# Performance work log

Measured on AMD Instinct MI355X. Metric: run time of the kernel, lower is better.

Reference implementation:

```python
import jax, jax.numpy as jnp
import numpy as np

N_HEADS = 32
N_KV_HEADS = 8
HEAD_DIM = 128
DIM = 4096
BSZ = 2
SEQLEN = 2048
ROPE_THETA = 500000.0


def setup_inputs() -> dict:
    key = jax.random.key(0)
    ks = jax.random.split(key, 6)
    s = 0.02
    x = jax.random.normal(ks[0], (BSZ, SEQLEN, DIM), dtype=jnp.float32)
    wq = jax.random.normal(ks[1], (N_HEADS * HEAD_DIM, DIM), dtype=jnp.float32) * s
    wk = jax.random.normal(ks[2], (N_KV_HEADS * HEAD_DIM, DIM), dtype=jnp.float32) * s
    wv = jax.random.normal(ks[3], (N_KV_HEADS * HEAD_DIM, DIM), dtype=jnp.float32) * s
    wo = jax.random.normal(ks[4], (DIM, N_HEADS * HEAD_DIM), dtype=jnp.float32) * s
    cache_k = jnp.zeros((BSZ, SEQLEN, N_KV_HEADS, HEAD_DIM), dtype=jnp.float32)
    cache_v = jnp.zeros((BSZ, SEQLEN, N_KV_HEADS, HEAD_DIM), dtype=jnp.float32)
    # rotary frequencies: freqs_cis[t, j] = exp(i * t * theta^(-2j/hd)); pass cos/sin parts
    inv = 1.0 / (ROPE_THETA ** (jnp.arange(0, HEAD_DIM, 2, dtype=jnp.float32) / HEAD_DIM))
    t = jnp.arange(SEQLEN, dtype=jnp.float32)
    ang = jnp.outer(t, inv)  # [S, hd/2]
    freqs_cos = jnp.cos(ang)
    freqs_sin = jnp.sin(ang)
    # causal additive mask
    mask = jnp.triu(jnp.full((SEQLEN, SEQLEN), -jnp.inf, dtype=jnp.float32), k=1)
    return {"x": x, "wq": wq, "wk": wk, "wv": wv, "wo": wo,
            "cache_k": cache_k, "cache_v": cache_v,
            "freqs_cos": freqs_cos, "freqs_sin": freqs_sin,
            "mask": mask, "start_pos": 0}


def _apply_rope(t, cos, sin):
    # t: [B, S, h, hd]; cos/sin: [S, hd/2]
    B, S, h, hd = t.shape
    tf = t.astype(jnp.float32).reshape(B, S, h, hd // 2, 2)
    a, b = tf[..., 0], tf[..., 1]
    c = cos[None, :, None, :]
    s = sin[None, :, None, :]
    out = jnp.stack([a * c - b * s, a * s + b * c], axis=-1)
    return out.reshape(B, S, h, hd).astype(t.dtype)


def reference(x, wq, wk, wv, wo, cache_k, cache_v, freqs_cos, freqs_sin, mask, start_pos):
    B, S, D = x.shape
    hd = HEAD_DIM
    n_rep = N_HEADS // N_KV_HEADS
    xq = (x @ wq.T).reshape(B, S, N_HEADS, hd)
    xk = (x @ wk.T).reshape(B, S, N_KV_HEADS, hd)
    xv = (x @ wv.T).reshape(B, S, N_KV_HEADS, hd)
    xq = _apply_rope(xq, freqs_cos, freqs_sin)
    xk = _apply_rope(xk, freqs_cos, freqs_sin)
    # KV cache write + slice
    cache_k = jax.lax.dynamic_update_slice(cache_k, xk, (0, start_pos, 0, 0))
    cache_v = jax.lax.dynamic_update_slice(cache_v, xv, (0, start_pos, 0, 0))
    kv_len = start_pos + S
    keys = cache_k[:B, :kv_len]    # [B, K, kvh, hd]
    values = cache_v[:B, :kv_len]
    # GQA: repeat kv heads
    keys = jnp.repeat(keys, n_rep, axis=2)     # [B, K, H, hd]
    values = jnp.repeat(values, n_rep, axis=2)
    q = xq.transpose(0, 2, 1, 3)       # [B, H, S, hd]
    k = keys.transpose(0, 2, 1, 3)     # [B, H, K, hd]
    v = values.transpose(0, 2, 1, 3)
    scores = jnp.einsum('bhqd,bhkd->bhqk', q, k) / jnp.sqrt(jnp.float32(hd))
    if mask is not None:
        scores = scores + mask[None, None, :, :]
    probs = jax.nn.softmax(scores.astype(jnp.float32), axis=-1).astype(q.dtype)
    out = jnp.einsum('bhqk,bhkd->bhqd', probs, v)
    out = out.transpose(0, 2, 1, 3).reshape(B, S, N_HEADS * hd)
    return out @ wo.T
```

## Files before the change

### kernel.cpp

```cpp
#include <hip/hip_runtime.h>
#include <hip/hip_bf16.h>
#include <math.h>

typedef __attribute__((ext_vector_type(8)))  __bf16 bfrag;
typedef __attribute__((ext_vector_type(4)))  float  f32x4;
typedef __attribute__((ext_vector_type(16))) float  f32x16;
typedef __attribute__((ext_vector_type(8)))  short  s16x8;
typedef __attribute__((ext_vector_type(4)))  short  s16x4;
typedef __attribute__((ext_vector_type(2)))  unsigned u32x2;
typedef __attribute__((ext_vector_type(4)))  unsigned u32x4;

__device__ __forceinline__ short f2bf(float f) {
  return (short)__builtin_bit_cast(unsigned short, (__bf16)f);
}
__device__ __forceinline__ float bf2f(short s) {
  return (float)__builtin_bit_cast(__bf16, (unsigned short)s);
}
__device__ __forceinline__ unsigned cvtpk(float lo, float hi_) {
  unsigned r;
  asm("v_cvt_pk_bf16_f32 %0, %1, %2" : "=v"(r) : "v"(lo), "v"(hi_));
  return r;
}
__device__ __forceinline__ void gll16(const void* g, void* l) {
  __builtin_amdgcn_global_load_lds((const __attribute__((address_space(1))) void*)g,
                                   (__attribute__((address_space(3))) void*)l, 16, 0, 0);
}

__global__ __launch_bounds__(256) void cvt_f32_bf16(const float* __restrict__ in,
                                                    short* __restrict__ out, int n4) {
  int i = blockIdx.x * 256 + threadIdx.x;
  if (i >= n4) return;
  f32x4 v = ((const f32x4*)in)[i];
  s16x4 o;
  o.x = f2bf(v.x); o.y = f2bf(v.y); o.z = f2bf(v.z); o.w = f2bf(v.w);
  ((s16x4*)out)[i] = o;
}

template<bool BF16OUT>
__global__ __launch_bounds__(512) void gemm256(const short* __restrict__ A,
                                               const short* __restrict__ B,
                                               void* __restrict__ Cv,
                                               int M, int N, int K, int NBX) {
  __shared__ __align__(16) short As[2][256 * 64];
  __shared__ __align__(16) short Bs[2][256 * 64];
  const int tid = threadIdx.x, lane = tid & 63, wid = tid >> 6;
  const int lr = lane & 15, lg = lane >> 4;
  const int wm = wid >> 2, wn = wid & 3;
  const int nwg = gridDim.x, orig = blockIdx.x;
  const int qq = nwg >> 3, rr = nwg & 7, xc = orig & 7, o8 = orig >> 3;
  const int wg = (xc < rr ? xc * (qq + 1) : rr * (qq + 1) + (xc - rr) * qq) + o8;
  const int bm = (wg / NBX) << 8, bn = (wg % NBX) << 8;
  const int NT = K >> 6;
  const int r0 = tid >> 3;
  const int c0 = tid & 7;
  const int csrc = c0 ^ (r0 & 7);

#define STG(OP, OPs, boff, bb, hh, kt_)                                          \
  do {                                                                           \
    _Pragma("unroll")                                                            \
    for (int s = 0; s < 2; ++s)                                                  \
      gll16(OP + (size_t)(boff + (hh) * 128 + s * 64 + r0) * K + (kt_) * 64 + csrc * 8, \
            (char*)OPs[bb] + ((hh) * 128 + s * 64 + wid * 8) * 128);             \
  } while (0)

  int ch[2];
#pragma unroll
  for (int ks = 0; ks < 2; ++ks) ch[ks] = (((ks << 2) | lg) ^ (lr & 7)) << 4;
  const int aoff = (wm * 128 + lr) * 128;
  const int boff_ = (wn * 64 + lr) * 128;

#define RD_A(dst, bb, ih)                                                        \
  do {                                                                           \
    const char* ab = (const char*)As[bb] + aoff + (ih) * 8192;                   \
    _Pragma("unroll") for (int i = 0; i < 4; ++i)                                \
      _Pragma("unroll") for (int ks = 0; ks < 2; ++ks)                           \
        dst[i][ks] = *(const bfrag*)(ab + i * 2048 + ch[ks]);                    \
  } while (0)
#define RD_B(dst, bb, jh)                                                        \
  do {                                                                           \
    const char* bp = (const char*)Bs[bb] + boff_ + (jh) * 4096;                  \
    _Pragma("unroll") for (int j = 0; j < 2; ++j)                                \
      _Pragma("unroll") for (int ks = 0; ks < 2; ++ks)                           \
        dst[j][ks] = *(const bfrag*)(bp + j * 2048 + ch[ks]);                    \
  } while (0)
#define MFMA16(af, bf, ih, jh)                                                   \
  do {                                                                           \
    __builtin_amdgcn_s_setprio(1);                                               \
    _Pragma("unroll") for (int i = 0; i < 4; ++i)                                \
      _Pragma("unroll") for (int j = 0; j < 2; ++j)                              \
        _Pragma("unroll") for (int ks = 0; ks < 2; ++ks)                         \
          acc[(ih) * 4 + i][(jh) * 2 + j] = __builtin_amdgcn_mfma_f32_16x16x32_bf16( \
              af[i][ks], bf[j][ks], acc[(ih) * 4 + i][(jh) * 2 + j], 0, 0, 0);   \
    __builtin_amdgcn_s_setprio(0);                                               \
  } while (0)

  STG(A, As, bm, 0, 0, 0); STG(A, As, bm, 0, 1, 0);
  STG(B, Bs, bn, 0, 0, 0); STG(B, Bs, bn, 0, 1, 0);
  if (NT > 1) {
    STG(B, Bs, bn, 1, 0, 1); STG(B, Bs, bn, 1, 1, 1);
    asm volatile("s_waitcnt vmcnt(4)" ::: "memory");
  } else {
    asm volatile("s_waitcnt vmcnt(0)" ::: "memory");
  }
  __builtin_amdgcn_s_barrier();
  __builtin_amdgcn_sched_barrier(0);

  f32x4 acc[8][4] = {};
  bfrag a_[4][2], b_lo[2][2], b_hi[2][2];

  for (int kt = 0; kt < NT; ++kt) {
    const int b = kt & 1;
    RD_A(a_, b, 0);
    RD_B(b_lo, b, 0);
    if (kt + 1 < NT) STG(A, As, bm, b ^ 1, 0, kt + 1);
    MFMA16(a_, b_lo, 0, 0);
    RD_B(b_hi, b, 1);
    if (kt + 1 < NT) STG(A, As, bm, b ^ 1, 1, kt + 1);
    MFMA16(a_, b_hi, 0, 1);
    __builtin_amdgcn_s_barrier();
    __builtin_amdgcn_sched_barrier(0);
    RD_A(a_, b, 1);
    if (kt + 2 < NT) STG(B, Bs, bn, b, 0, kt + 2);
    MFMA16(a_, b_hi, 1, 1);
    if (kt + 2 < NT) STG(B, Bs, bn, b, 1, kt + 2);
    MFMA16(a_, b_lo, 1, 0);
    if (kt + 1 < NT) {
      if (kt + 2 < NT) asm volatile("s_waitcnt vmcnt(4)" ::: "memory");
      else             asm volatile("s_waitcnt vmcnt(0)" ::: "memory");
      __builtin_amdgcn_s_barrier();
      __builtin_amdgcn_sched_barrier(0);
    }
  }
#undef STG
#undef RD_A
#undef RD_B
#undef MFMA16
  const int rb = bm + wm * 128 + lg * 4, cb = bn + wn * 64 + lr;
#pragma unroll
  for (int i = 0; i < 8; ++i)
#pragma unroll
    for (int j = 0; j < 4; ++j)
#pragma unroll
      for (int r = 0; r < 4; ++r) {
        size_t idx = (size_t)(rb + i * 16 + r) * N + (cb + j * 16);
        if (BF16OUT) ((short*)Cv)[idx] = f2bf(acc[i][j][r]);
        else         ((float*)Cv)[idx] = acc[i][j][r];
      }
}

__global__ __launch_bounds__(256) void rope_k(short* __restrict__ qkv,
                                              const float* __restrict__ fcos,
                                              const float* __restrict__ fsin) {
  const int t = blockIdx.x;
  const int s = t & 2047;
  unsigned* row = (unsigned*)(qkv + (size_t)t * 6144);
  for (int p = threadIdx.x; p < 2560; p += 256) {
    const int h = p >> 6, i = p & 63;
    const int w = h * 64 + i;
    unsigned u = row[w];
    float a  = bf2f((short)(u & 0xffff));
    float b  = bf2f((short)(u >> 16));
    float c  = fcos[s * 64 + i], sn = fsin[s * 64 + i];
    float na = a * c - b * sn;
    float nb = a * sn + b * c;
    row[w] = ((unsigned)(unsigned short)f2bf(na)) |
             (((unsigned)(unsigned short)f2bf(nb)) << 16);
  }
}

__global__ __launch_bounds__(256) void vtrans(const short* __restrict__ qkv,
                                              short* __restrict__ vt) {
  const int sb = blockIdx.x, kvh = blockIdx.y, b = blockIdx.z;
  __shared__ short T[64][136];
  const int tid = threadIdx.x;
#pragma unroll
  for (int it = 0; it < 4; ++it) {
    int c = it * 256 + tid;
    int r = c >> 4, dc = c & 15;
    s16x8 v = *(const s16x8*)(qkv + (size_t)(b * 2048 + sb * 64 + r) * 6144
                              + 5120 + kvh * 128 + dc * 8);
    *(s16x8*)&T[r][dc * 8] = v;
  }
  __syncthreads();
#pragma unroll
  for (int it = 0; it < 4; ++it) {
    int c = it * 256 + tid;
    int d = c >> 3, sc = c & 7;
    s16x8 v;
#pragma unroll
    for (int j = 0; j < 8; ++j) v[j] = T[sc * 8 + j][d];
    *(s16x8*)(vt + (size_t)((b * 8 + kvh) * 128 + d) * 2048 + sb * 64 + sc * 8) = v;
  }
}

__global__ __launch_bounds__(512, 2) void fattn2(const short* __restrict__ qkv,
                                                 const short* __restrict__ vt,
                                                 short* __restrict__ ao) {
  const int qb = blockIdx.x, h = blockIdx.y, b = blockIdx.z;
  const int kvh = h >> 2;
  const int tid = threadIdx.x;
  const int lane = tid & 63, wid = tid >> 6;
  const int l31 = lane & 31, hi = lane >> 5;
  __shared__ __align__(16) short Ks[2][64 * 128];
  __shared__ __align__(16) short Vs[2][128 * 64];

  const int q0w   = qb * 256 + wid * 32;
  const int qg    = q0w + l31;
  const int tmaxw = q0w >> 6;
  const int NT    = 4 * qb + 4;

  bfrag qf[8];
  {
    const short* qp = qkv + (size_t)(b * 2048 + qg) * 6144 + h * 128 + hi * 8;
#pragma unroll
    for (int kk = 0; kk < 8; ++kk) qf[kk] = *(const bfrag*)(qp + kk * 16);
  }

  const int kr0 = tid >> 4, kcc = tid & 15;
  const int vd0 = tid >> 3, vkc = tid & 7;
  const int kro[2] = { kr0, kr0 + 32 };
  const int vdo[2] = { vd0, vd0 + 64 };
  int kldst[2], vldst[2];
#pragma unroll
  for (int i = 0; i < 2; ++i) {
    kldst[i] = (kro[i] * 256 + kcc * 16) ^ ((kro[i] & 7) << 4);
    vldst[i] = (vdo[i] * 128 + vkc * 16) ^ ((vdo[i] & 7) << 4);
  }
  const short* base_k = qkv + (size_t)(b * 2048) * 6144 + 4096 + kvh * 128;
  const short* base_v = vt + (size_t)((b * 8 + kvh) * 128) * 2048;

  {
    s16x8 kr_[2], vr_[2];
#pragma unroll
    for (int i = 0; i < 2; ++i) {
      kr_[i] = *(const s16x8*)(base_k + (size_t)kro[i] * 6144 + kcc * 8);
      vr_[i] = *(const s16x8*)(base_v + (size_t)vdo[i] * 2048 + vkc * 8);
    }
#pragma unroll
    for (int i = 0; i < 2; ++i) {
      *(s16x8*)((char*)Ks[0] + kldst[i]) = kr_[i];
      *(s16x8*)((char*)Vs[0] + vldst[i]) = vr_[i];
    }
  }
  __syncthreads();

  f32x16 o[4] = {};
  float m = -3.0e38f, l = 0.f;
  const float c0 = 0.08838834764831845f * 1.4426950408889634f;
  const int  sw = (l31 & 7) << 4;

  for (int t = 0; t < NT; ++t) {
    const int cur = t & 1;
    s16x8 kr_[2], vr_[2];
    const bool pf = (t + 1 < NT);
    if (pf) {
#pragma unroll
      for (int i = 0; i < 2; ++i) {
        kr_[i] = *(const s16x8*)(base_k + (size_t)((t + 1) * 64 + kro[i]) * 6144 + kcc * 8);
        vr_[i] = *(const s16x8*)(base_v + (size_t)vdo[i] * 2048 + (t + 1) * 64 + vkc * 8);
      }
    }
    if (t <= tmaxw) {
      f32x16 st[2];
      __builtin_amdgcn_s_setprio(1);
#pragma unroll
      for (int kt = 0; kt < 2; ++kt) {
        f32x16 acc = {};
        const char* kb = (const char*)Ks[cur] + kt * 8192 + l31 * 256;
#pragma unroll
        for (int kk = 0; kk < 8; ++kk) {
          bfrag kf = *(const bfrag*)(kb + ((kk * 32 + hi * 16) ^ sw));
          acc = __builtin_amdgcn_mfma_f32_32x32x16_bf16(kf, qf[kk], acc, 0, 0, 0);
        }
        st[kt] = acc;
      }
      __builtin_amdgcn_s_setprio(0);
      if (t == tmaxw) {
        const int kb0 = t * 64 + 4 * hi;
#pragma unroll
        for (int kt = 0; kt < 2; ++kt)
#pragma unroll
          for (int r = 0; r < 16; ++r) {
            int k = kb0 + kt * 32 + (r & 3) + 8 * (r >> 2);
            if (k > qg) st[kt][r] = -3.0e38f;
          }
      }
      float mt = -3.0e38f;
#pragma unroll
      for (int kt = 0; kt < 2; ++kt)
#pragma unroll
        for (int r = 0; r < 16; ++r) mt = fmaxf(mt, st[kt][r]);
      mt = fmaxf(mt, __shfl_xor(mt, 32, 64));
      if (!__all((mt - m) * c0 <= 8.0f)) {
        float nm = fmaxf(m, mt);
        float fe = exp2f((m - nm) * c0);
        m = nm;
        l *= fe;
#pragma unroll
        for (int dt = 0; dt < 4; ++dt)
#pragma unroll
          for (int r = 0; r < 16; ++r) o[dt][r] *= fe;
      }
      const float mc = m * c0;
      float ps = 0.f;
#pragma unroll
      for (int kt = 0; kt < 2; ++kt)
#pragma unroll
        for (int r = 0; r < 16; ++r) {
          float p = exp2f(st[kt][r] * c0 - mc);
          st[kt][r] = p;
          ps += p;
        }
      ps += __shfl_xor(ps, 32, 64);
      l += ps;
      bfrag pfr[4];
#pragma unroll
      for (int kt = 0; kt < 2; ++kt) {
        u32x2 a0 = __builtin_amdgcn_permlane32_swap(cvtpk(st[kt][0],  st[kt][1]),
                                                    cvtpk(st[kt][4],  st[kt][5]),  0, 0);
        u32x2 a1 = __builtin_amdgcn_permlane32_swap(cvtpk(st[kt][2],  st[kt][3]),
                                                    cvtpk(st[kt][6],  st[kt][7]),  0, 0);
        u32x2 b0 = __builtin_amdgcn_permlane32_swap(cvtpk(st[kt][8],  st[kt][9]),
                                                    cvtpk(st[kt][12], st[kt][13]), 0, 0);
        u32x2 b1 = __builtin_amdgcn_permlane32_swap(cvtpk(st[kt][10], st[kt][11]),
                                                    cvtpk(st[kt][14], st[kt][15]), 0, 0);
        u32x4 w0 = { a0.x, a1.x, a0.y, a1.y };
        u32x4 w1 = { b0.x, b1.x, b0.y, b1.y };
        pfr[kt * 2]     = __builtin_bit_cast(bfrag, w0);
        pfr[kt * 2 + 1] = __builtin_bit_cast(bfrag, w1);
      }
      __builtin_amdgcn_s_setprio(1);
#pragma unroll
      for (int ks = 0; ks < 4; ++ks) {
        const char* vb = (const char*)Vs[cur] + l31 * 128 + ((ks * 32 + hi * 16) ^ sw);
#pragma unroll
        for (int dt = 0; dt < 4; ++dt) {
          bfrag vf = *(const bfrag*)(vb + dt * 4096);
          o[dt] = __builtin_amdgcn_mfma_f32_32x32x16_bf16(vf, pfr[ks], o[dt], 0, 0, 0);
        }
      }
      __builtin_amdgcn_s_setprio(0);
    }
    __syncthreads();
    if (pf) {
#pragma unroll
      for (int i = 0; i < 2; ++i) {
        *(s16x8*)((char*)Ks[cur ^ 1] + kldst[i]) = kr_[i];
        *(s16x8*)((char*)Vs[cur ^ 1] + vldst[i]) = vr_[i];
      }
    }
    __syncthreads();
  }
  const float linv = 1.f / l;
  short* aop = ao + (size_t)(b * 2048 + qg) * 4096 + h * 128 + 4 * hi;
#pragma unroll
  for (int dt = 0; dt < 4; ++dt)
#pragma unroll
    for (int r = 0; r < 16; ++r) {
      int d = dt * 32 + (r & 3) + 8 * (r >> 2);
      aop[d] = f2bf(o[dt][r] * linv);
    }
}

extern "C" void kernel_launch(void* const* d_in, const int* in_sizes, int n_in,
                              void* d_out, int out_size, void* d_ws, size_t ws_size,
                              hipStream_t stream) {
  const float* x  = (const float*)d_in[0];
  const float* wq = (const float*)d_in[1];
  const float* wk = (const float*)d_in[2];
  const float* wv = (const float*)d_in[3];
  const float* wo = (const float*)d_in[4];
  const float* fc = (const float*)d_in[7];
  const float* fs = (const float*)d_in[8];

  char* ws = (char*)d_ws;
  short* xb    = (short*)(ws);
  short* ao    = xb;
  short* wqkvb = (short*)(ws + 33554432ull);
  short* wob   = wqkvb;
  short* qkv   = (short*)(ws + 83886080ull);
  short* vt    = (short*)(ws + 134217728ull);

  cvt_f32_bf16<<<16384, 256, 0, stream>>>(x,  xb,                 4194304);
  cvt_f32_bf16<<<16384, 256, 0, stream>>>(wq, wqkvb,              4194304);
  cvt_f32_bf16<<< 4096, 256, 0, stream>>>(wk, wqkvb + 16777216,   1048576);
  cvt_f32_bf16<<< 4096, 256, 0, stream>>>(wv, wqkvb + 20971520,   1048576);
  gemm256<true ><<<384, 512, 0, stream>>>(xb, wqkvb, qkv, 4096, 6144, 4096, 24);
  rope_k<<<4096, 256, 0, stream>>>(qkv, fc, fs);
  vtrans<<<dim3(32, 8, 2), 256, 0, stream>>>(qkv, vt);
  fattn2<<<dim3(8, 32, 2), 512, 0, stream>>>(qkv, vt, ao);
  cvt_f32_bf16<<<16384, 256, 0, stream>>>(wo, wob,                4194304);
  gemm256<false><<<256, 512, 0, stream>>>(ao, wob, (float*)d_out, 4096, 4096, 4096, 16);
}
```

Measured before the change: 586.6 us.

## Shrink GEMM tiles to 128x128 with 256 threads and restructure prefetch pipeline

Replaces the 256x256-tile, 512-thread GEMM with a 128x128-tile, 256-thread variant for both the QKV and output projections. The grid grows from 384/256 blocks to 1536/1024, which fills the 256 CUs more evenly and lowers the LDS and register footprint per block so more blocks can be resident. The global-to-LDS staging order and vmcnt waits are reworked to prefetch A and B a stage ahead with the new split. In exchange, each tile reuses its operands less, which raises global/L2 traffic per FLOP.

```diff
diff --git a/kernel.cpp b/kernel.cpp
--- a/kernel.cpp
+++ b/kernel.cpp
@@ -37,19 +37,19 @@
 }
 
 template<bool BF16OUT>
-__global__ __launch_bounds__(512) void gemm256(const short* __restrict__ A,
+__global__ __launch_bounds__(256) void gemm128(const short* __restrict__ A,
                                                const short* __restrict__ B,
                                                void* __restrict__ Cv,
                                                int M, int N, int K, int NBX) {
-  __shared__ __align__(16) short As[2][256 * 64];
-  __shared__ __align__(16) short Bs[2][256 * 64];
+  __shared__ __align__(16) short As[2][128 * 64];
+  __shared__ __align__(16) short Bs[2][128 * 64];
   const int tid = threadIdx.x, lane = tid & 63, wid = tid >> 6;
   const int lr = lane & 15, lg = lane >> 4;
-  const int wm = wid >> 2, wn = wid & 3;
+  const int wm = wid >> 1, wn = wid & 1;
   const int nwg = gridDim.x, orig = blockIdx.x;
   const int qq = nwg >> 3, rr = nwg & 7, xc = orig & 7, o8 = orig >> 3;
   const int wg = (xc < rr ? xc * (qq + 1) : rr * (qq + 1) + (xc - rr) * qq) + o8;
-  const int bm = (wg / NBX) << 8, bn = (wg % NBX) << 8;
+  const int bm = (wg / NBX) << 7, bn = (wg % NBX) << 7;
   const int NT = K >> 6;
   const int r0 = tid >> 3;
   const int c0 = tid & 7;
@@ -59,73 +59,72 @@
   do {                                                                           \
     _Pragma("unroll")                                                            \
     for (int s = 0; s < 2; ++s)                                                  \
-      gll16(OP + (size_t)(boff + (hh) * 128 + s * 64 + r0) * K + (kt_) * 64 + csrc * 8, \
-            (char*)OPs[bb] + ((hh) * 128 + s * 64 + wid * 8) * 128);             \
+      gll16(OP + (size_t)(boff + (hh) * 64 + s * 32 + r0) * K + (kt_) * 64 + csrc * 8, \
+            (char*)OPs[bb] + ((hh) * 64 + s * 32 + wid * 8) * 128);              \
   } while (0)
 
   int ch[2];
 #pragma unroll
   for (int ks = 0; ks < 2; ++ks) ch[ks] = (((ks << 2) | lg) ^ (lr & 7)) << 4;
-  const int aoff = (wm * 128 + lr) * 128;
-  const int boff_ = (wn * 64 + lr) * 128;
-
-#define RD_A(dst, bb, ih)                                                        \
+  const int aoff  = (wm * 64 + lr) * 128;
+  const int boff2 = (wn * 32 + lr) * 128;
+
+#define RD_A(dst, bb)                                                            \
   do {                                                                           \
-    const char* ab = (const char*)As[bb] + aoff + (ih) * 8192;                   \
+    const char* ab = (const char*)As[bb] + aoff;                                 \
     _Pragma("unroll") for (int i = 0; i < 4; ++i)                                \
       _Pragma("unroll") for (int ks = 0; ks < 2; ++ks)                           \
         dst[i][ks] = *(const bfrag*)(ab + i * 2048 + ch[ks]);                    \
   } while (0)
 #define RD_B(dst, bb, jh)                                                        \
   do {                                                                           \
-    const char* bp = (const char*)Bs[bb] + boff_ + (jh) * 4096;                  \
+    const char* bp = (const char*)Bs[bb] + boff2 + (jh) * 8192;                  \
     _Pragma("unroll") for (int j = 0; j < 2; ++j)                                \
       _Pragma("unroll") for (int ks = 0; ks < 2; ++ks)                           \
         dst[j][ks] = *(const bfrag*)(bp + j * 2048 + ch[ks]);                    \
   } while (0)
-#define MFMA16(af, bf, ih, jh)                                                   \
+#define MFMA16(af, bf, jh)                                                       \
   do {                                                                           \
     __builtin_amdgcn_s_setprio(1);                                               \
     _Pragma("unroll") for (int i = 0; i < 4; ++i)                                \
       _Pragma("unroll") for (int j = 0; j < 2; ++j)                              \
         _Pragma("unroll") for (int ks = 0; ks < 2; ++ks)                         \
-          acc[(ih) * 4 + i][(jh) * 2 + j] = __builtin_amdgcn_mfma_f32_16x16x32_bf16( \
-              af[i][ks], bf[j][ks], acc[(ih) * 4 + i][(jh) * 2 + j], 0, 0, 0);   \
+          acc[i][(jh) * 2 + j] = __builtin_amdgcn_mfma_f32_16x16x32_bf16(        \
+              af[i][ks], bf[j][ks], acc[i][(jh) * 2 + j], 0, 0, 0);              \
     __builtin_amdgcn_s_setprio(0);                                               \
   } while (0)
 
   STG(A, As, bm, 0, 0, 0); STG(A, As, bm, 0, 1, 0);
   STG(B, Bs, bn, 0, 0, 0); STG(B, Bs, bn, 0, 1, 0);
   if (NT > 1) {
-    STG(B, Bs, bn, 1, 0, 1); STG(B, Bs, bn, 1, 1, 1);
-    asm volatile("s_waitcnt vmcnt(4)" ::: "memory");
+    STG(A, As, bm, 1, 0, 1); STG(A, As, bm, 1, 1, 1);
+    STG(B, Bs, bn, 1, 0, 1);
+    asm volatile("s_waitcnt vmcnt(6)" ::: "memory");
   } else {
     asm volatile("s_waitcnt vmcnt(0)" ::: "memory");
   }
   __builtin_amdgcn_s_barrier();
   __builtin_amdgcn_sched_barrier(0);
 
-  f32x4 acc[8][4] = {};
+  f32x4 acc[4][4] = {};
   bfrag a_[4][2], b_lo[2][2], b_hi[2][2];
 
   for (int kt = 0; kt < NT; ++kt) {
     const int b = kt & 1;
-    RD_A(a_, b, 0);
+    RD_A(a_, b);
     RD_B(b_lo, b, 0);
-    if (kt + 1 < NT) STG(A, As, bm, b ^ 1, 0, kt + 1);
-    MFMA16(a_, b_lo, 0, 0);
-    RD_B(b_hi, b, 1);
-    if (kt + 1 < NT) STG(A, As, bm, b ^ 1, 1, kt + 1);
-    MFMA16(a_, b_hi, 0, 1);
+    if (kt + 1 < NT) STG(B, Bs, bn, b ^ 1, 1, kt + 1);
+    MFMA16(a_, b_lo, 0);
     __builtin_amdgcn_s_barrier();
     __builtin_amdgcn_sched_barrier(0);
-    RD_A(a_, b, 1);
-    if (kt + 2 < NT) STG(B, Bs, bn, b, 0, kt + 2);
-    MFMA16(a_, b_hi, 1, 1);
-    if (kt + 2 < NT) STG(B, Bs, bn, b, 1, kt + 2);
-    MFMA16(a_, b_lo, 1, 0);
+    RD_B(b_hi, b, 1);
+    if (kt + 2 < NT) {
+      STG(A, As, bm, b, 0, kt + 2); STG(A, As, bm, b, 1, kt + 2);
+      STG(B, Bs, bn, b, 0, kt + 2);
+    }
+    MFMA16(a_, b_hi, 1);
     if (kt + 1 < NT) {
-      if (kt + 2 < NT) asm volatile("s_waitcnt vmcnt(4)" ::: "memory");
+      if (kt + 2 < NT) asm volatile("s_waitcnt vmcnt(6)" ::: "memory");
       else             asm volatile("s_waitcnt vmcnt(0)" ::: "memory");
       __builtin_amdgcn_s_barrier();
       __builtin_amdgcn_sched_barrier(0);
@@ -135,17 +134,19 @@
 #undef RD_A
 #undef RD_B
 #undef MFMA16
-  const int rb = bm + wm * 128 + lg * 4, cb = bn + wn * 64 + lr;
-#pragma unroll
-  for (int i = 0; i < 8; ++i)
-#pragma unroll
-    for (int j = 0; j < 4; ++j)
-#pragma unroll
-      for (int r = 0; r < 4; ++r) {
-        size_t idx = (size_t)(rb + i * 16 + r) * N + (cb + j * 16);
-        if (BF16OUT) ((short*)Cv)[idx] = f2bf(acc[i][j][r]);
-        else         ((float*)Cv)[idx] = acc[i][j][r];
-      }
+  const int rb = bm + wm * 64 + lg * 4, cb = bn + wn * 32 + lr;
+#pragma unroll
+  for (int i = 0; i < 4; ++i)
+#pragma unroll
+    for (int jh = 0; jh < 2; ++jh)
+#pragma unroll
+      for (int j = 0; j < 2; ++j)
+#pragma unroll
+        for (int r = 0; r < 4; ++r) {
+          size_t idx = (size_t)(rb + i * 16 + r) * N + (cb + jh * 64 + j * 16);
+          if (BF16OUT) ((short*)Cv)[idx] = f2bf(acc[i][jh * 2 + j][r]);
+          else         ((float*)Cv)[idx] = acc[i][jh * 2 + j][r];
+        }
 }
 
 __global__ __launch_bounds__(256) void rope_k(short* __restrict__ qkv,
@@ -385,10 +386,10 @@
   cvt_f32_bf16<<<16384, 256, 0, stream>>>(wq, wqkvb,              4194304);
   cvt_f32_bf16<<< 4096, 256, 0, stream>>>(wk, wqkvb + 16777216,   1048576);
   cvt_f32_bf16<<< 4096, 256, 0, stream>>>(wv, wqkvb + 20971520,   1048576);
-  gemm256<true ><<<384, 512, 0, stream>>>(xb, wqkvb, qkv, 4096, 6144, 4096, 24);
+  gemm128<true ><<<1536, 256, 0, stream>>>(xb, wqkvb, qkv, 4096, 6144, 4096, 48);
   rope_k<<<4096, 256, 0, stream>>>(qkv, fc, fs);
   vtrans<<<dim3(32, 8, 2), 256, 0, stream>>>(qkv, vt);
   fattn2<<<dim3(8, 32, 2), 512, 0, stream>>>(qkv, vt, ao);
   cvt_f32_bf16<<<16384, 256, 0, stream>>>(wo, wob,                4194304);
-  gemm256<false><<<256, 512, 0, stream>>>(ao, wob, (float*)d_out, 4096, 4096, 4096, 16);
-}
+  gemm128<false><<<1024, 256, 0, stream>>>(ao, wob, (float*)d_out, 4096, 4096, 4096, 32);
+}
```

New measurement: 618.6 us. +5.4%, slower.
